# Kernel tuning notes

Measured on AMD Instinct MI355X. Metric: run time of the kernel, lower is better.

## Reference

```python
import jax, jax.numpy as jnp
import numpy as np

IN_F, OUT_F, RANK = 4096, 4096, 64
ALPHA = 128.0
SCALING = ALPHA / RANK  # 2.0
BATCH_TOKENS = 8192


def setup_inputs() -> dict:
    key = jax.random.key(0)
    k1, k2, k3, k4 = jax.random.split(key, 4)
    x = jax.random.normal(k1, (BATCH_TOKENS, IN_F), dtype=jnp.float32)
    weight = jax.random.normal(k2, (OUT_F, IN_F), dtype=jnp.float32) * 0.02
    P = jax.random.normal(k3, (OUT_F, RANK), dtype=jnp.float32) * 0.01
    Lambda = jnp.ones((RANK,), dtype=jnp.float32) * 0.01
    Q = jax.random.normal(k4, (RANK, IN_F), dtype=jnp.float32) * 0.01
    rank_mask = jnp.ones((RANK,), dtype=jnp.bool_)
    return {"x": x, "weight": weight, "P": P, "Lambda": Lambda, "Q": Q, "rank_mask": rank_mask}


def reference(x, weight, P, Lambda, Q, rank_mask):
    # active_Lambda = Lambda * mask; delta_W = (P * active_Lambda) @ Q  -> [OUT_F, IN_F]
    active_Lambda = Lambda * rank_mask.astype(Lambda.dtype)
    delta_W = (P * active_Lambda[None, :]) @ Q
    # F.linear(x, W_eff) = x @ W_eff^T
    W_eff = weight + SCALING * delta_W
    return x @ W_eff.T
```

## Files before the change

### kernel.cpp

```cpp
#include <hip/hip_runtime.h>
#include <hip/hip_bf16.h>
#include <stdint.h>

#define M_TOK 8192
#define NF    4096
#define KF    4096
#define RANK  64

typedef __attribute__((ext_vector_type(8))) short short8;
typedef __attribute__((ext_vector_type(4))) float floatx4;

typedef const uint32_t __attribute__((address_space(1)))* gp1_t;
typedef uint32_t __attribute__((address_space(3)))* lp3_t;

__device__ __forceinline__ void load_lds16(const void* g, void* l) {
  __builtin_amdgcn_global_load_lds((gp1_t)g, (lp3_t)l, 16, 0, 0);
}

__global__ void cast_f32_bf16(const float* __restrict__ in,
                              __hip_bfloat16* __restrict__ out) {
  size_t i = ((size_t)blockIdx.x * blockDim.x + threadIdx.x) * 8;
  float4 a = *(const float4*)(in + i);
  float4 b = *(const float4*)(in + i + 4);
  union { __hip_bfloat16 h[8]; uint4 u; } pk;
  pk.h[0] = __float2bfloat16(a.x);
  pk.h[1] = __float2bfloat16(a.y);
  pk.h[2] = __float2bfloat16(a.z);
  pk.h[3] = __float2bfloat16(a.w);
  pk.h[4] = __float2bfloat16(b.x);
  pk.h[5] = __float2bfloat16(b.y);
  pk.h[6] = __float2bfloat16(b.z);
  pk.h[7] = __float2bfloat16(b.w);
  *(uint4*)(out + i) = pk.u;
}

__global__ __launch_bounds__(256) void build_weff(
    const float* __restrict__ W, const float* __restrict__ P,
    const float* __restrict__ Lam, const float* __restrict__ Q,
    const unsigned char* __restrict__ mask,
    __hip_bfloat16* __restrict__ Wb) {
  __shared__ float lam[RANK];
  __shared__ float plT[RANK][68];
  __shared__ float Qs[RANK][68];

  const int t = threadIdx.x;
  const int n0 = blockIdx.y * 64;
  const int k0 = blockIdx.x * 64;

  if (t < RANK) lam[t] = 2.0f * Lam[t] * (mask[t] ? 1.0f : 0.0f);
  __syncthreads();

  {
    const int nl = t & 63;
    const int rg = (t >> 6) * 16;
    const float* p = P + (size_t)(n0 + nl) * RANK + rg;
#pragma unroll
    for (int j = 0; j < 16; j += 4) {
      float4 v = *(const float4*)(p + j);
      plT[rg + j + 0][nl] = v.x * lam[rg + j + 0];
      plT[rg + j + 1][nl] = v.y * lam[rg + j + 1];
      plT[rg + j + 2][nl] = v.z * lam[rg + j + 2];
      plT[rg + j + 3][nl] = v.w * lam[rg + j + 3];
    }
    const int r = t >> 2;
    const int kc = (t & 3) * 16;
    const float* q = Q + (size_t)r * KF + k0 + kc;
#pragma unroll
    for (int j = 0; j < 16; j += 4) {
      float4 v = *(const float4*)(q + j);
      Qs[r][kc + j + 0] = v.x;
      Qs[r][kc + j + 1] = v.y;
      Qs[r][kc + j + 2] = v.z;
      Qs[r][kc + j + 3] = v.w;
    }
  }
  __syncthreads();

  const int tn4 = t >> 4;
  const int tk4 = t & 15;
  float accv[4][4];
#pragma unroll
  for (int i = 0; i < 4; i++) {
    float4 w = *(const float4*)(W + (size_t)(n0 + tn4 * 4 + i) * KF + k0 + tk4 * 4);
    accv[i][0] = w.x; accv[i][1] = w.y; accv[i][2] = w.z; accv[i][3] = w.w;
  }
#pragma unroll 8
  for (int r = 0; r < RANK; r++) {
    float4 p4 = *(const float4*)&plT[r][tn4 * 4];
    float4 q4 = *(const float4*)&Qs[r][tk4 * 4];
#define ROWFMA(i, pi)                                                  \
    accv[i][0] += (pi) * q4.x; accv[i][1] += (pi) * q4.y;              \
    accv[i][2] += (pi) * q4.z; accv[i][3] += (pi) * q4.w;
    ROWFMA(0, p4.x) ROWFMA(1, p4.y) ROWFMA(2, p4.z) ROWFMA(3, p4.w)
#undef ROWFMA
  }
#pragma unroll
  for (int i = 0; i < 4; i++) {
    union { __hip_bfloat16 h[4]; uint2 u; } pk;
    pk.h[0] = __float2bfloat16(accv[i][0]);
    pk.h[1] = __float2bfloat16(accv[i][1]);
    pk.h[2] = __float2bfloat16(accv[i][2]);
    pk.h[3] = __float2bfloat16(accv[i][3]);
    *(uint2*)(Wb + (size_t)(n0 + tn4 * 4 + i) * KF + k0 + tk4 * 4) = pk.u;
  }
}

#define BM 256
#define BN 256
#define BK 64
#define NT (KF / BK)
#define ASL 16384

__device__ __forceinline__ void read_a4(short8 (&afr)[2][2],
                                        const __hip_bfloat16* Asl,
                                        int row_base, int swz) {
#pragma unroll
  for (int mm = 0; mm < 2; ++mm)
#pragma unroll
    for (int ks = 0; ks < 2; ++ks)
      afr[mm][ks] = *(const short8*)(Asl + ks * 8192 + (row_base + mm * 16) * 32 + swz);
}

template <int P>
__device__ __forceinline__ void mfma16(floatx4 (&acc)[8][4],
                                       const short8 (&afr)[2][2],
                                       const short8 (&bfr)[4][2]) {
#pragma unroll
  for (int ks = 0; ks < 2; ++ks)
#pragma unroll
    for (int mm = 0; mm < 2; ++mm)
#pragma unroll
      for (int nf = 0; nf < 4; ++nf)
        acc[P * 2 + mm][nf] = __builtin_amdgcn_mfma_f32_16x16x32_bf16(
            afr[mm][ks], bfr[nf][ks], acc[P * 2 + mm][nf], 0, 0, 0);
}

__global__ __launch_bounds__(512, 2) void gemm_xwt(
    const __hip_bfloat16* __restrict__ A,
    const __hip_bfloat16* __restrict__ B,
    float* __restrict__ C) {
  extern __shared__ __hip_bfloat16 lds[];
  __hip_bfloat16* As = lds;
  __hip_bfloat16* Bs = lds + 2 * ASL;

  const int t = threadIdx.x;
  const int lane = t & 63;
  const int wave = t >> 6;
  const int wm = wave >> 2;
  const int wn = wave & 3;
  const int frow = lane & 15;
  const int kq = lane >> 4;
  const int swz = ((kq + (frow >> 1)) & 3) * 8;

  const int bid = blockIdx.x;
  const int wk = (bid & 7) * 64 + (bid >> 3);
  const int bm = wk >> 4;
  const int bn = wk & 15;

  const int c = ((t & 3) - ((t >> 3) & 3)) & 3;
  const __hip_bfloat16* a_src = A + (size_t)(bm * BM + (t >> 2)) * KF + c * 8;
  const __hip_bfloat16* b_src = B + (size_t)(bn * BN + (t >> 2)) * KF + c * 8;
  __hip_bfloat16* a_dst = As + t * 8;
  __hip_bfloat16* b_dst = Bs + t * 8;

#define STAGE_A(kt_, slot_, h_)                                                        \
  do {                                                                                 \
    const __hip_bfloat16* s_ = a_src + ((kt_) & (NT - 1)) * BK + (size_t)(h_) * 128 * KF; \
    __hip_bfloat16* d_ = a_dst + (slot_) * ASL + (h_) * 4096;                          \
    load_lds16(s_, d_);                                                \
    load_lds16(s_ + 32, d_ + 8192);                                    \
  } while (0)
#define STAGE_B(kt_, slot_, h_)                                                        \
  do {                                                                                 \
    const __hip_bfloat16* s_ = b_src + ((kt_) & (NT - 1)) * BK + (size_t)(h_) * 128 * KF; \
    __hip_bfloat16* d_ = b_dst + (slot_) * ASL + (h_) * 4096;                          \
    load_lds16(s_, d_);                                                                \
    load_lds16(s_ + 32, d_ + 8192);                                                    \
  } while (0)

  floatx4 acc[8][4] = {};

  STAGE_A(0, 0, 0); STAGE_A(0, 0, 1);
  STAGE_B(0, 0, 0); STAGE_B(0, 0, 1);
  STAGE_B(1, 1, 0); STAGE_B(1, 1, 1);
  asm volatile("s_waitcnt vmcnt(4)" ::: "memory");
  __builtin_amdgcn_s_barrier();

  const int arow = wm * 128 + frow;
  const int brow = wn * 64 + frow;

  for (int kt = 0; kt < NT; ++kt) {
    const int cur = kt & 1;
    const __hip_bfloat16* Asl = As + cur * ASL;
    const __hip_bfloat16* Bsl = Bs + cur * ASL;

    short8 bfr[4][2];
    short8 afr[2][2];

#pragma unroll
    for (int nf = 0; nf < 4; ++nf)
#pragma unroll
      for (int ks = 0; ks < 2; ++ks)
        bfr[nf][ks] = *(const short8*)(Bsl + ks * 8192 + (brow + nf * 16) * 32 + swz);
    read_a4(afr, Asl, arow + 0 * 32, swz);
    STAGE_A(kt + 1, cur ^ 1, 0);
    __builtin_amdgcn_sched_barrier(0);
    __builtin_amdgcn_s_barrier();
    asm volatile("s_waitcnt lgkmcnt(0)" ::: "memory");
    __builtin_amdgcn_sched_barrier(0);
    __builtin_amdgcn_s_setprio(1);
    mfma16<0>(acc, afr, bfr);
    __builtin_amdgcn_s_setprio(0);
    __builtin_amdgcn_sched_barrier(0);
    __builtin_amdgcn_s_barrier();

    read_a4(afr, Asl, arow + 1 * 32, swz);
    STAGE_A(kt + 1, cur ^ 1, 1);
    __builtin_amdgcn_sched_barrier(0);
    __builtin_amdgcn_s_barrier();
    asm volatile("s_waitcnt lgkmcnt(0)" ::: "memory");
    __builtin_amdgcn_sched_barrier(0);
    __builtin_amdgcn_s_setprio(1);
    mfma16<1>(acc, afr, bfr);
    __builtin_amdgcn_s_setprio(0);
    __builtin_amdgcn_sched_barrier(0);
    __builtin_amdgcn_s_barrier();

    read_a4(afr, Asl, arow + 2 * 32, swz);
    STAGE_B(kt + 2, cur, 0);
    __builtin_amdgcn_sched_barrier(0);
    __builtin_amdgcn_s_barrier();
    asm volatile("s_waitcnt lgkmcnt(0)" ::: "memory");
    __builtin_amdgcn_sched_barrier(0);
    __builtin_amdgcn_s_setprio(1);
    mfma16<2>(acc, afr, bfr);
    __builtin_amdgcn_s_setprio(0);
    __builtin_amdgcn_sched_barrier(0);
    __builtin_amdgcn_s_barrier();

    read_a4(afr, Asl, arow + 3 * 32, swz);
    STAGE_B(kt + 2, cur, 1);
    __builtin_amdgcn_sched_barrier(0);
    __builtin_amdgcn_s_barrier();
    asm volatile("s_waitcnt lgkmcnt(0)" ::: "memory");
    __builtin_amdgcn_sched_barrier(0);
    __builtin_amdgcn_s_setprio(1);
    mfma16<3>(acc, afr, bfr);
    __builtin_amdgcn_s_setprio(0);
    __builtin_amdgcn_sched_barrier(0);
    asm volatile("s_waitcnt vmcnt(4)" ::: "memory");
    __builtin_amdgcn_s_barrier();
  }

#undef STAGE_A
#undef STAGE_B

  const int col0 = bn * BN + wn * 64 + (lane & 15);
  const int row0 = bm * BM + wm * 128 + (lane >> 4) * 4;
#pragma unroll
  for (int mf = 0; mf < 8; ++mf)
#pragma unroll
    for (int nf = 0; nf < 4; ++nf)
#pragma unroll
      for (int r = 0; r < 4; ++r)
        C[(size_t)(row0 + mf * 16 + r) * NF + (col0 + nf * 16)] = acc[mf][nf][r];
}

extern "C" void kernel_launch(void* const* d_in, const int* in_sizes, int n_in,
                              void* d_out, int out_size, void* d_ws, size_t ws_size,
                              hipStream_t stream) {
  const float* x      = (const float*)d_in[0];
  const float* weight = (const float*)d_in[1];
  const float* P      = (const float*)d_in[2];
  const float* Lam    = (const float*)d_in[3];
  const float* Q      = (const float*)d_in[4];
  const unsigned char* mask = (const unsigned char*)d_in[5];
  float* out = (float*)d_out;

  __hip_bfloat16* Xb = (__hip_bfloat16*)d_ws;
  __hip_bfloat16* Wb = (__hip_bfloat16*)((char*)d_ws + (size_t)M_TOK * KF * 2);

  static int smem_set = 0;
  if (!smem_set) {
    hipFuncSetAttribute((const void*)gemm_xwt,
                        hipFuncAttributeMaxDynamicSharedMemorySize, 131072);
    smem_set = 1;
  }

  cast_f32_bf16<<<(M_TOK * KF) / (256 * 8), 256, 0, stream>>>(x, Xb);
  build_weff<<<dim3(KF / 64, NF / 64), 256, 0, stream>>>(weight, P, Lam, Q, mask, Wb);
  gemm_xwt<<<dim3((M_TOK / BM) * (NF / BN)), 512, 131072, stream>>>(Xb, Wb, out);
}
```

Baseline: 514.0 us.

## Apply low-rank update as X·Qᵀ·Vᵀ epilogue instead of building W_eff

```diff
diff --git a/kernel.cpp b/kernel.cpp
--- a/kernel.cpp
+++ b/kernel.cpp
@@ -34,75 +34,69 @@
   *(uint4*)(out + i) = pk.u;
 }
 
-__global__ __launch_bounds__(256) void build_weff(
-    const float* __restrict__ W, const float* __restrict__ P,
-    const float* __restrict__ Lam, const float* __restrict__ Q,
-    const unsigned char* __restrict__ mask,
-    __hip_bfloat16* __restrict__ Wb) {
-  __shared__ float lam[RANK];
-  __shared__ float plT[RANK][68];
-  __shared__ float Qs[RANK][68];
-
+__global__ __launch_bounds__(256) void prep_qv(
+    const float* __restrict__ Q, const float* __restrict__ P,
+    const float* __restrict__ Lam, const unsigned char* __restrict__ mask,
+    __hip_bfloat16* __restrict__ Qb, __hip_bfloat16* __restrict__ Vb) {
+  int idx = blockIdx.x * 256 + threadIdx.x;
+  if (idx < (RANK * KF) / 8) {
+    size_t i = (size_t)idx * 8;
+    float4 a = *(const float4*)(Q + i);
+    float4 b = *(const float4*)(Q + i + 4);
+    union { __hip_bfloat16 h[8]; uint4 u; } pk;
+    pk.h[0] = __float2bfloat16(a.x); pk.h[1] = __float2bfloat16(a.y);
+    pk.h[2] = __float2bfloat16(a.z); pk.h[3] = __float2bfloat16(a.w);
+    pk.h[4] = __float2bfloat16(b.x); pk.h[5] = __float2bfloat16(b.y);
+    pk.h[6] = __float2bfloat16(b.z); pk.h[7] = __float2bfloat16(b.w);
+    *(uint4*)(Qb + i) = pk.u;
+  } else {
+    idx -= (RANK * KF) / 8;
+    size_t i = (size_t)idx * 8;
+    const int rb = (int)(i & (RANK - 1));
+    float4 a = *(const float4*)(P + i);
+    float4 b = *(const float4*)(P + i + 4);
+    float s[8];
+#pragma unroll
+    for (int j = 0; j < 8; ++j)
+      s[j] = 2.0f * Lam[rb + j] * (mask[rb + j] ? 1.0f : 0.0f);
+    union { __hip_bfloat16 h[8]; uint4 u; } pk;
+    pk.h[0] = __float2bfloat16(a.x * s[0]); pk.h[1] = __float2bfloat16(a.y * s[1]);
+    pk.h[2] = __float2bfloat16(a.z * s[2]); pk.h[3] = __float2bfloat16(a.w * s[3]);
+    pk.h[4] = __float2bfloat16(b.x * s[4]); pk.h[5] = __float2bfloat16(b.y * s[5]);
+    pk.h[6] = __float2bfloat16(b.z * s[6]); pk.h[7] = __float2bfloat16(b.w * s[7]);
+    *(uint4*)(Vb + i) = pk.u;
+  }
+}
+
+__global__ __launch_bounds__(128) void gemm_xqt(
+    const __hip_bfloat16* __restrict__ X,
+    const __hip_bfloat16* __restrict__ Qb,
+    __hip_bfloat16* __restrict__ U) {
   const int t = threadIdx.x;
-  const int n0 = blockIdx.y * 64;
-  const int k0 = blockIdx.x * 64;
-
-  if (t < RANK) lam[t] = 2.0f * Lam[t] * (mask[t] ? 1.0f : 0.0f);
-  __syncthreads();
-
-  {
-    const int nl = t & 63;
-    const int rg = (t >> 6) * 16;
-    const float* p = P + (size_t)(n0 + nl) * RANK + rg;
-#pragma unroll
-    for (int j = 0; j < 16; j += 4) {
-      float4 v = *(const float4*)(p + j);
-      plT[rg + j + 0][nl] = v.x * lam[rg + j + 0];
-      plT[rg + j + 1][nl] = v.y * lam[rg + j + 1];
-      plT[rg + j + 2][nl] = v.z * lam[rg + j + 2];
-      plT[rg + j + 3][nl] = v.w * lam[rg + j + 3];
+  const int lane = t & 63;
+  const int w = t >> 6;
+  const int frow = lane & 15;
+  const int kq = lane >> 4;
+  const int m0 = blockIdx.x * 32 + w * 16;
+  const __hip_bfloat16* xp = X + (size_t)(m0 + frow) * KF + kq * 8;
+  floatx4 acc[4] = {};
+#pragma unroll 4
+  for (int k0 = 0; k0 < KF; k0 += 32) {
+    short8 af = *(const short8*)(xp + k0);
+#pragma unroll
+    for (int nf = 0; nf < 4; ++nf) {
+      short8 bf = *(const short8*)(Qb + (size_t)(nf * 16 + frow) * KF + k0 + kq * 8);
+      acc[nf] = __builtin_amdgcn_mfma_f32_16x16x32_bf16(af, bf, acc[nf], 0, 0, 0);
     }
-    const int r = t >> 2;
-    const int kc = (t & 3) * 16;
-    const float* q = Q + (size_t)r * KF + k0 + kc;
-#pragma unroll
-    for (int j = 0; j < 16; j += 4) {
-      float4 v = *(const float4*)(q + j);
-      Qs[r][kc + j + 0] = v.x;
-      Qs[r][kc + j + 1] = v.y;
-      Qs[r][kc + j + 2] = v.z;
-      Qs[r][kc + j + 3] = v.w;
-    }
-  }
-  __syncthreads();
-
-  const int tn4 = t >> 4;
-  const int tk4 = t & 15;
-  float accv[4][4];
-#pragma unroll
-  for (int i = 0; i < 4; i++) {
-    float4 w = *(const float4*)(W + (size_t)(n0 + tn4 * 4 + i) * KF + k0 + tk4 * 4);
-    accv[i][0] = w.x; accv[i][1] = w.y; accv[i][2] = w.z; accv[i][3] = w.w;
-  }
-#pragma unroll 8
-  for (int r = 0; r < RANK; r++) {
-    float4 p4 = *(const float4*)&plT[r][tn4 * 4];
-    float4 q4 = *(const float4*)&Qs[r][tk4 * 4];
-#define ROWFMA(i, pi)                                                  \
-    accv[i][0] += (pi) * q4.x; accv[i][1] += (pi) * q4.y;              \
-    accv[i][2] += (pi) * q4.z; accv[i][3] += (pi) * q4.w;
-    ROWFMA(0, p4.x) ROWFMA(1, p4.y) ROWFMA(2, p4.z) ROWFMA(3, p4.w)
-#undef ROWFMA
-  }
-#pragma unroll
-  for (int i = 0; i < 4; i++) {
-    union { __hip_bfloat16 h[4]; uint2 u; } pk;
-    pk.h[0] = __float2bfloat16(accv[i][0]);
-    pk.h[1] = __float2bfloat16(accv[i][1]);
-    pk.h[2] = __float2bfloat16(accv[i][2]);
-    pk.h[3] = __float2bfloat16(accv[i][3]);
-    *(uint2*)(Wb + (size_t)(n0 + tn4 * 4 + i) * KF + k0 + tk4 * 4) = pk.u;
-  }
+  }
+  const int col = lane & 15;
+  const int r0 = (lane >> 4) * 4;
+#pragma unroll
+  for (int nf = 0; nf < 4; ++nf)
+#pragma unroll
+    for (int r = 0; r < 4; ++r)
+      U[(size_t)(m0 + r0 + r) * RANK + nf * 16 + col] =
+          __float2bfloat16(acc[nf][r]);
 }
 
 #define BM 256
@@ -111,6 +105,10 @@
 #define NT (KF / BK)
 #define ASL 16384
 
+#define SB0 __builtin_amdgcn_sched_barrier(0)
+#define BARSYNC do { SB0; __builtin_amdgcn_s_barrier(); } while (0)
+#define LGK(n) do { asm volatile("s_waitcnt lgkmcnt(" #n ")" ::: "memory"); SB0; } while (0)
+
 __device__ __forceinline__ void read_a4(short8 (&afr)[2][2],
                                         const __hip_bfloat16* Asl,
                                         int row_base, int swz) {
@@ -119,6 +117,16 @@
 #pragma unroll
     for (int ks = 0; ks < 2; ++ks)
       afr[mm][ks] = *(const short8*)(Asl + ks * 8192 + (row_base + mm * 16) * 32 + swz);
+}
+
+__device__ __forceinline__ void read_b8(short8 (&bfr)[4][2],
+                                        const __hip_bfloat16* Bsl,
+                                        int brow, int swz) {
+#pragma unroll
+  for (int nf = 0; nf < 4; ++nf)
+#pragma unroll
+    for (int ks = 0; ks < 2; ++ks)
+      bfr[nf][ks] = *(const short8*)(Bsl + ks * 8192 + (brow + nf * 16) * 32 + swz);
 }
 
 template <int P>
@@ -138,10 +146,16 @@
 __global__ __launch_bounds__(512, 2) void gemm_xwt(
     const __hip_bfloat16* __restrict__ A,
     const __hip_bfloat16* __restrict__ B,
+    const __hip_bfloat16* __restrict__ U,
+    const __hip_bfloat16* __restrict__ V,
     float* __restrict__ C) {
   extern __shared__ __hip_bfloat16 lds[];
   __hip_bfloat16* As = lds;
   __hip_bfloat16* Bs = lds + 2 * ASL;
+  const __hip_bfloat16* As0 = As;
+  const __hip_bfloat16* As1 = As + ASL;
+  const __hip_bfloat16* Bs0 = Bs;
+  const __hip_bfloat16* Bs1 = Bs + ASL;
 
   const int t = threadIdx.x;
   const int lane = t & 63;
@@ -179,81 +193,98 @@
   } while (0)
 
   floatx4 acc[8][4] = {};
+  short8 bE[4][2], bO[4][2];
+  short8 aX[2][2], aY[2][2];
+
+  const int arow = wm * 128 + frow;
+  const int brow = wn * 64 + frow;
 
   STAGE_A(0, 0, 0); STAGE_A(0, 0, 1);
   STAGE_B(0, 0, 0); STAGE_B(0, 0, 1);
   STAGE_B(1, 1, 0); STAGE_B(1, 1, 1);
   asm volatile("s_waitcnt vmcnt(4)" ::: "memory");
   __builtin_amdgcn_s_barrier();
-
-  const int arow = wm * 128 + frow;
-  const int brow = wn * 64 + frow;
-
-  for (int kt = 0; kt < NT; ++kt) {
-    const int cur = kt & 1;
-    const __hip_bfloat16* Asl = As + cur * ASL;
-    const __hip_bfloat16* Bsl = Bs + cur * ASL;
-
-    short8 bfr[4][2];
-    short8 afr[2][2];
-
-#pragma unroll
-    for (int nf = 0; nf < 4; ++nf)
-#pragma unroll
-      for (int ks = 0; ks < 2; ++ks)
-        bfr[nf][ks] = *(const short8*)(Bsl + ks * 8192 + (brow + nf * 16) * 32 + swz);
-    read_a4(afr, Asl, arow + 0 * 32, swz);
-    STAGE_A(kt + 1, cur ^ 1, 0);
-    __builtin_amdgcn_sched_barrier(0);
+  read_b8(bE, Bs0, brow, swz);
+  read_a4(aX, As0, arow + 0 * 32, swz);
+
+  for (int kt = 0; kt < NT; kt += 2) {
+    read_a4(aY, As0, arow + 1 * 32, swz);
+    STAGE_A(kt + 1, 1, 0);
+    BARSYNC; LGK(4);
+    __builtin_amdgcn_s_setprio(1); mfma16<0>(acc, aX, bE); __builtin_amdgcn_s_setprio(0);
+    BARSYNC;
+    read_a4(aX, As0, arow + 2 * 32, swz);
+    STAGE_A(kt + 1, 1, 1);
+    BARSYNC; LGK(4);
+    __builtin_amdgcn_s_setprio(1); mfma16<1>(acc, aY, bE); __builtin_amdgcn_s_setprio(0);
+    BARSYNC;
+    read_a4(aY, As0, arow + 3 * 32, swz);
+    STAGE_B(kt + 2, 0, 0);
+    BARSYNC; LGK(4);
+    __builtin_amdgcn_s_setprio(1); mfma16<2>(acc, aX, bE); __builtin_amdgcn_s_setprio(0);
+    SB0;
+    asm volatile("s_waitcnt vmcnt(2)" ::: "memory");
     __builtin_amdgcn_s_barrier();
-    asm volatile("s_waitcnt lgkmcnt(0)" ::: "memory");
-    __builtin_amdgcn_sched_barrier(0);
-    __builtin_amdgcn_s_setprio(1);
-    mfma16<0>(acc, afr, bfr);
-    __builtin_amdgcn_s_setprio(0);
-    __builtin_amdgcn_sched_barrier(0);
+    read_b8(bO, Bs1, brow, swz);
+    read_a4(aX, As1, arow + 0 * 32, swz);
+    STAGE_B(kt + 2, 0, 1);
+    BARSYNC; LGK(12);
+    __builtin_amdgcn_s_setprio(1); mfma16<3>(acc, aY, bE); __builtin_amdgcn_s_setprio(0);
+    BARSYNC;
+
+    read_a4(aY, As1, arow + 1 * 32, swz);
+    STAGE_A(kt + 2, 0, 0);
+    BARSYNC; LGK(4);
+    __builtin_amdgcn_s_setprio(1); mfma16<0>(acc, aX, bO); __builtin_amdgcn_s_setprio(0);
+    BARSYNC;
+    read_a4(aX, As1, arow + 2 * 32, swz);
+    STAGE_A(kt + 2, 0, 1);
+    BARSYNC; LGK(4);
+    __builtin_amdgcn_s_setprio(1); mfma16<1>(acc, aY, bO); __builtin_amdgcn_s_setprio(0);
+    BARSYNC;
+    read_a4(aY, As1, arow + 3 * 32, swz);
+    STAGE_B(kt + 3, 1, 0);
+    BARSYNC; LGK(4);
+    __builtin_amdgcn_s_setprio(1); mfma16<2>(acc, aX, bO); __builtin_amdgcn_s_setprio(0);
+    SB0;
+    asm volatile("s_waitcnt vmcnt(2)" ::: "memory");
     __builtin_amdgcn_s_barrier();
-
-    read_a4(afr, Asl, arow + 1 * 32, swz);
-    STAGE_A(kt + 1, cur ^ 1, 1);
-    __builtin_amdgcn_sched_barrier(0);
-    __builtin_amdgcn_s_barrier();
-    asm volatile("s_waitcnt lgkmcnt(0)" ::: "memory");
-    __builtin_amdgcn_sched_barrier(0);
-    __builtin_amdgcn_s_setprio(1);
-    mfma16<1>(acc, afr, bfr);
-    __builtin_amdgcn_s_setprio(0);
-    __builtin_amdgcn_sched_barrier(0);
-    __builtin_amdgcn_s_barrier();
-
-    read_a4(afr, Asl, arow + 2 * 32, swz);
-    STAGE_B(kt + 2, cur, 0);
-    __builtin_amdgcn_sched_barrier(0);
-    __builtin_amdgcn_s_barrier();
-    asm volatile("s_waitcnt lgkmcnt(0)" ::: "memory");
-    __builtin_amdgcn_sched_barrier(0);
-    __builtin_amdgcn_s_setprio(1);
-    mfma16<2>(acc, afr, bfr);
-    __builtin_amdgcn_s_setprio(0);
-    __builtin_amdgcn_sched_barrier(0);
-    __builtin_amdgcn_s_barrier();
-
-    read_a4(afr, Asl, arow + 3 * 32, swz);
-    STAGE_B(kt + 2, cur, 1);
-    __builtin_amdgcn_sched_barrier(0);
-    __builtin_amdgcn_s_barrier();
-    asm volatile("s_waitcnt lgkmcnt(0)" ::: "memory");
-    __builtin_amdgcn_sched_barrier(0);
-    __builtin_amdgcn_s_setprio(1);
-    mfma16<3>(acc, afr, bfr);
-    __builtin_amdgcn_s_setprio(0);
-    __builtin_amdgcn_sched_barrier(0);
-    asm volatile("s_waitcnt vmcnt(4)" ::: "memory");
-    __builtin_amdgcn_s_barrier();
+    read_b8(bE, Bs0, brow, swz);
+    read_a4(aX, As0, arow + 0 * 32, swz);
+    STAGE_B(kt + 3, 1, 1);
+    BARSYNC; LGK(12);
+    __builtin_amdgcn_s_setprio(1); mfma16<3>(acc, aY, bO); __builtin_amdgcn_s_setprio(0);
+    BARSYNC;
   }
 
 #undef STAGE_A
 #undef STAGE_B
+
+  {
+    short8 vf[4][2];
+#pragma unroll
+    for (int nf = 0; nf < 4; ++nf)
+#pragma unroll
+      for (int ks = 0; ks < 2; ++ks)
+        vf[nf][ks] = *(const short8*)(V + (size_t)(bn * BN + wn * 64 + nf * 16 + frow) * RANK + ks * 32 + kq * 8);
+#pragma unroll
+    for (int p = 0; p < 4; ++p) {
+      short8 uf[2][2];
+#pragma unroll
+      for (int mm = 0; mm < 2; ++mm)
+#pragma unroll
+        for (int ks = 0; ks < 2; ++ks)
+          uf[mm][ks] = *(const short8*)(U + (size_t)(bm * BM + wm * 128 + p * 32 + mm * 16 + frow) * RANK + ks * 32 + kq * 8);
+#pragma unroll
+      for (int ks = 0; ks < 2; ++ks)
+#pragma unroll
+        for (int mm = 0; mm < 2; ++mm)
+#pragma unroll
+          for (int nf = 0; nf < 4; ++nf)
+            acc[p * 2 + mm][nf] = __builtin_amdgcn_mfma_f32_16x16x32_bf16(
+                uf[mm][ks], vf[nf][ks], acc[p * 2 + mm][nf], 0, 0, 0);
+    }
+  }
 
   const int col0 = bn * BN + wn * 64 + (lane & 15);
   const int row0 = bm * BM + wm * 128 + (lane >> 4) * 4;
@@ -277,8 +308,12 @@
   const unsigned char* mask = (const unsigned char*)d_in[5];
   float* out = (float*)d_out;
 
-  __hip_bfloat16* Xb = (__hip_bfloat16*)d_ws;
-  __hip_bfloat16* Wb = (__hip_bfloat16*)((char*)d_ws + (size_t)M_TOK * KF * 2);
+  char* ws = (char*)d_ws;
+  __hip_bfloat16* Xb = (__hip_bfloat16*)ws;
+  __hip_bfloat16* Wb = (__hip_bfloat16*)(ws + (size_t)M_TOK * KF * 2);
+  __hip_bfloat16* Qb = (__hip_bfloat16*)(ws + 96ull * 1024 * 1024);
+  __hip_bfloat16* Vb = (__hip_bfloat16*)(ws + 96ull * 1024 * 1024 + (size_t)RANK * KF * 2);
+  __hip_bfloat16* Ub = (__hip_bfloat16*)(ws + 97ull * 1024 * 1024);
 
   static int smem_set = 0;
   if (!smem_set) {
@@ -288,6 +323,8 @@
   }
 
   cast_f32_bf16<<<(M_TOK * KF) / (256 * 8), 256, 0, stream>>>(x, Xb);
-  build_weff<<<dim3(KF / 64, NF / 64), 256, 0, stream>>>(weight, P, Lam, Q, mask, Wb);
-  gemm_xwt<<<dim3((M_TOK / BM) * (NF / BN)), 512, 131072, stream>>>(Xb, Wb, out);
-}
+  cast_f32_bf16<<<(NF * KF) / (256 * 8), 256, 0, stream>>>(weight, Wb);
+  prep_qv<<<256, 256, 0, stream>>>(Q, P, Lam, mask, Qb, Vb);
+  gemm_xqt<<<M_TOK / 32, 128, 0, stream>>>(Xb, Qb, Ub);
+  gemm_xwt<<<dim3((M_TOK / BM) * (NF / BN)), 512, 131072, stream>>>(Xb, Wb, Ub, Vb, out);
+}
```

Result: slower. 554.7 us (+7.9%).

## Software-pipeline LDS fragment reads with double-buffered registers in GEMM main loop

Applied to the files above, without the earlier changes.

```diff
diff --git a/kernel.cpp b/kernel.cpp
--- a/kernel.cpp
+++ b/kernel.cpp
@@ -111,6 +111,10 @@
 #define NT (KF / BK)
 #define ASL 16384
 
+#define SB0 __builtin_amdgcn_sched_barrier(0)
+#define BARSYNC do { SB0; __builtin_amdgcn_s_barrier(); } while (0)
+#define LGK(n) do { asm volatile("s_waitcnt lgkmcnt(" #n ")" ::: "memory"); SB0; } while (0)
+
 __device__ __forceinline__ void read_a4(short8 (&afr)[2][2],
                                         const __hip_bfloat16* Asl,
                                         int row_base, int swz) {
@@ -119,6 +123,16 @@
 #pragma unroll
     for (int ks = 0; ks < 2; ++ks)
       afr[mm][ks] = *(const short8*)(Asl + ks * 8192 + (row_base + mm * 16) * 32 + swz);
+}
+
+__device__ __forceinline__ void read_b8(short8 (&bfr)[4][2],
+                                        const __hip_bfloat16* Bsl,
+                                        int brow, int swz) {
+#pragma unroll
+  for (int nf = 0; nf < 4; ++nf)
+#pragma unroll
+    for (int ks = 0; ks < 2; ++ks)
+      bfr[nf][ks] = *(const short8*)(Bsl + ks * 8192 + (brow + nf * 16) * 32 + swz);
 }
 
 template <int P>
@@ -142,6 +156,10 @@
   extern __shared__ __hip_bfloat16 lds[];
   __hip_bfloat16* As = lds;
   __hip_bfloat16* Bs = lds + 2 * ASL;
+  const __hip_bfloat16* As0 = As;
+  const __hip_bfloat16* As1 = As + ASL;
+  const __hip_bfloat16* Bs0 = Bs;
+  const __hip_bfloat16* Bs1 = Bs + ASL;
 
   const int t = threadIdx.x;
   const int lane = t & 63;
@@ -179,77 +197,68 @@
   } while (0)
 
   floatx4 acc[8][4] = {};
+  short8 bE[4][2], bO[4][2];
+  short8 aX[2][2], aY[2][2];
+
+  const int arow = wm * 128 + frow;
+  const int brow = wn * 64 + frow;
 
   STAGE_A(0, 0, 0); STAGE_A(0, 0, 1);
   STAGE_B(0, 0, 0); STAGE_B(0, 0, 1);
   STAGE_B(1, 1, 0); STAGE_B(1, 1, 1);
   asm volatile("s_waitcnt vmcnt(4)" ::: "memory");
   __builtin_amdgcn_s_barrier();
-
-  const int arow = wm * 128 + frow;
-  const int brow = wn * 64 + frow;
-
-  for (int kt = 0; kt < NT; ++kt) {
-    const int cur = kt & 1;
-    const __hip_bfloat16* Asl = As + cur * ASL;
-    const __hip_bfloat16* Bsl = Bs + cur * ASL;
-
-    short8 bfr[4][2];
-    short8 afr[2][2];
-
-#pragma unroll
-    for (int nf = 0; nf < 4; ++nf)
-#pragma unroll
-      for (int ks = 0; ks < 2; ++ks)
-        bfr[nf][ks] = *(const short8*)(Bsl + ks * 8192 + (brow + nf * 16) * 32 + swz);
-    read_a4(afr, Asl, arow + 0 * 32, swz);
-    STAGE_A(kt + 1, cur ^ 1, 0);
-    __builtin_amdgcn_sched_barrier(0);
+  read_b8(bE, Bs0, brow, swz);
+  read_a4(aX, As0, arow + 0 * 32, swz);
+
+  for (int kt = 0; kt < NT; kt += 2) {
+    read_a4(aY, As0, arow + 1 * 32, swz);
+    STAGE_A(kt + 1, 1, 0);
+    BARSYNC; LGK(4);
+    __builtin_amdgcn_s_setprio(1); mfma16<0>(acc, aX, bE); __builtin_amdgcn_s_setprio(0);
+    BARSYNC;
+    read_a4(aX, As0, arow + 2 * 32, swz);
+    STAGE_A(kt + 1, 1, 1);
+    BARSYNC; LGK(4);
+    __builtin_amdgcn_s_setprio(1); mfma16<1>(acc, aY, bE); __builtin_amdgcn_s_setprio(0);
+    BARSYNC;
+    read_a4(aY, As0, arow + 3 * 32, swz);
+    STAGE_B(kt + 2, 0, 0);
+    BARSYNC; LGK(4);
+    __builtin_amdgcn_s_setprio(1); mfma16<2>(acc, aX, bE); __builtin_amdgcn_s_setprio(0);
+    SB0;
+    asm volatile("s_waitcnt vmcnt(2)" ::: "memory");
     __builtin_amdgcn_s_barrier();
-    asm volatile("s_waitcnt lgkmcnt(0)" ::: "memory");
-    __builtin_amdgcn_sched_barrier(0);
-    __builtin_amdgcn_s_setprio(1);
-    mfma16<0>(acc, afr, bfr);
-    __builtin_amdgcn_s_setprio(0);
-    __builtin_amdgcn_sched_barrier(0);
+    read_b8(bO, Bs1, brow, swz);
+    read_a4(aX, As1, arow + 0 * 32, swz);
+    STAGE_B(kt + 2, 0, 1);
+    BARSYNC; LGK(12);
+    __builtin_amdgcn_s_setprio(1); mfma16<3>(acc, aY, bE); __builtin_amdgcn_s_setprio(0);
+    BARSYNC;
+
+    read_a4(aY, As1, arow + 1 * 32, swz);
+    STAGE_A(kt + 2, 0, 0);
+    BARSYNC; LGK(4);
+    __builtin_amdgcn_s_setprio(1); mfma16<0>(acc, aX, bO); __builtin_amdgcn_s_setprio(0);
+    BARSYNC;
+    read_a4(aX, As1, arow + 2 * 32, swz);
+    STAGE_A(kt + 2, 0, 1);
+    BARSYNC; LGK(4);
+    __builtin_amdgcn_s_setprio(1); mfma16<1>(acc, aY, bO); __builtin_amdgcn_s_setprio(0);
+    BARSYNC;
+    read_a4(aY, As1, arow + 3 * 32, swz);
+    STAGE_B(kt + 3, 1, 0);
+    BARSYNC; LGK(4);
+    __builtin_amdgcn_s_setprio(1); mfma16<2>(acc, aX, bO); __builtin_amdgcn_s_setprio(0);
+    SB0;
+    asm volatile("s_waitcnt vmcnt(2)" ::: "memory");
     __builtin_amdgcn_s_barrier();
-
-    read_a4(afr, Asl, arow + 1 * 32, swz);
-    STAGE_A(kt + 1, cur ^ 1, 1);
-    __builtin_amdgcn_sched_barrier(0);
-    __builtin_amdgcn_s_barrier();
-    asm volatile("s_waitcnt lgkmcnt(0)" ::: "memory");
-    __builtin_amdgcn_sched_barrier(0);
-    __builtin_amdgcn_s_setprio(1);
-    mfma16<1>(acc, afr, bfr);
-    __builtin_amdgcn_s_setprio(0);
-    __builtin_amdgcn_sched_barrier(0);
-    __builtin_amdgcn_s_barrier();
-
-    read_a4(afr, Asl, arow + 2 * 32, swz);
-    STAGE_B(kt + 2, cur, 0);
-    __builtin_amdgcn_sched_barrier(0);
-    __builtin_amdgcn_s_barrier();
-    asm volatile("s_waitcnt lgkmcnt(0)" ::: "memory");
-    __builtin_amdgcn_sched_barrier(0);
-    __builtin_amdgcn_s_setprio(1);
-    mfma16<2>(acc, afr, bfr);
-    __builtin_amdgcn_s_setprio(0);
-    __builtin_amdgcn_sched_barrier(0);
-    __builtin_amdgcn_s_barrier();
-
-    read_a4(afr, Asl, arow + 3 * 32, swz);
-    STAGE_B(kt + 2, cur, 1);
-    __builtin_amdgcn_sched_barrier(0);
-    __builtin_amdgcn_s_barrier();
-    asm volatile("s_waitcnt lgkmcnt(0)" ::: "memory");
-    __builtin_amdgcn_sched_barrier(0);
-    __builtin_amdgcn_s_setprio(1);
-    mfma16<3>(acc, afr, bfr);
-    __builtin_amdgcn_s_setprio(0);
-    __builtin_amdgcn_sched_barrier(0);
-    asm volatile("s_waitcnt vmcnt(4)" ::: "memory");
-    __builtin_amdgcn_s_barrier();
+    read_b8(bE, Bs0, brow, swz);
+    read_a4(aX, As0, arow + 0 * 32, swz);
+    STAGE_B(kt + 3, 1, 1);
+    BARSYNC; LGK(12);
+    __builtin_amdgcn_s_setprio(1); mfma16<3>(acc, aY, bO); __builtin_amdgcn_s_setprio(0);
+    BARSYNC;
   }
 
 #undef STAGE_A
```

After: 531.8 us. +3.5%, slower.
